# Kernel tuning notes

Measured on AMD Instinct MI355X. Metric: run time of the kernel, lower is better.

## Reference

```python
import jax, jax.numpy as jnp
import numpy as np

D_MODEL = 64     # input_dim // 4
D_INNER = 128    # expand * d_model
D_STATE = 16
D_CONV = 4
DT_RANK = 4      # ceil(d_model / 16)
EPS = 1e-5


def layernorm(x, g, b):
    m = x.mean(-1, keepdims=True)
    v = x.var(-1, keepdims=True)
    return (x - m) * jax.lax.rsqrt(v + EPS) * g + b


def mamba(u, W_in, W_conv, b_conv, W_xproj, W_dt, b_dt, A_log, Dp, W_out):
    # u: [B, L, d_model]
    B, L, _ = u.shape
    xz = u @ W_in.T                              # [B, L, 2*d_inner]
    xi, z = xz[..., :D_INNER], xz[..., D_INNER:]
    # depthwise causal conv1d over L
    xp = jnp.pad(xi, ((0, 0), (D_CONV - 1, 0), (0, 0)))
    xc = b_conv + sum(xp[:, k:k + L, :] * W_conv[:, k] for k in range(D_CONV))
    xc = jax.nn.silu(xc)                         # [B, L, d_inner]
    proj = xc @ W_xproj.T                        # [B, L, dt_rank + 2*d_state]
    dtp = proj[..., :DT_RANK]
    Bm = proj[..., DT_RANK:DT_RANK + D_STATE]    # [B, L, d_state]
    Cm = proj[..., DT_RANK + D_STATE:]           # [B, L, d_state]
    dt = jax.nn.softplus(dtp @ W_dt.T + b_dt)    # [B, L, d_inner]
    A = -jnp.exp(A_log)                          # [d_inner, d_state]
    dA = jnp.exp(dt[..., None] * A)              # [B, L, d_inner, d_state]
    dBx = (dt * xc)[..., None] * Bm[:, :, None, :]

    def step(h, t):
        dA_t, dBx_t, C_t = t
        h = dA_t * h + dBx_t                     # [B, d_inner, d_state]
        return h, jnp.einsum('bds,bs->bd', h, C_t)

    h0 = jnp.zeros((B, D_INNER, D_STATE), u.dtype)
    _, ys = jax.lax.scan(step, h0, (dA.transpose(1, 0, 2, 3),
                                    dBx.transpose(1, 0, 2, 3),
                                    Cm.transpose(1, 0, 2)))
    y = ys.transpose(1, 0, 2) + Dp * xc          # [B, L, d_inner]
    y = y * jax.nn.silu(z)
    return y @ W_out.T                           # [B, L, d_model]


def _forward(x, x1, x2, x3, g1, be1, g2, be2, g3, be3, g4, be4, skip_scale,
             W_in, W_conv, b_conv, W_xproj, W_dt, b_dt, A_log, D, W_out):
    Bb, C = x.shape[:2]
    img_dims = x2.shape[2:]
    mparams = (W_in, W_conv, b_conv, W_xproj, W_dt, b_dt, A_log, D, W_out)

    def branch(inp, g, b):
        xf = inp.reshape(Bb, C, -1).transpose(0, 2, 1)   # [B, L, C]
        xn = layernorm(xf, g, b)
        return mamba(xn, *mparams) + skip_scale * xn

    x_mamba = jnp.concatenate([branch(x, g1, be1), branch(x1, g2, be2),
                               branch(x2, g3, be3), branch(x3, g4, be4)], axis=2)
    out = x_mamba.transpose(0, 2, 1).reshape(Bb, 4 * C, *img_dims)
    return out


def setup_inputs():
    key = jax.random.key(0)
    ks = jax.random.split(key, 12)
    f = lambda k, shp, s=1.0: jax.random.normal(k, shp, dtype=jnp.float32) * s
    inp = {
        'x': f(ks[0], (8, 64, 32, 32)),
        'x1': f(ks[1], (8, 64, 32, 32)),
        'x2': f(ks[2], (8, 64, 32, 32)),
        'x3': f(ks[3], (8, 64, 32, 32)),
        'g1': jnp.ones(64), 'be1': jnp.zeros(64),
        'g2': jnp.ones(64), 'be2': jnp.zeros(64),
        'g3': jnp.ones(64), 'be3': jnp.zeros(64),
        'g4': jnp.ones(64), 'be4': jnp.zeros(64),
        'skip_scale': jnp.ones((1,), jnp.float32),
        'W_in': f(ks[4], (2 * D_INNER, D_MODEL), 0.1),
        'W_conv': f(ks[5], (D_INNER, D_CONV), 0.3),
        'b_conv': jnp.zeros(D_INNER),
        'W_xproj': f(ks[6], (DT_RANK + 2 * D_STATE, D_INNER), 0.1),
        'W_dt': f(ks[7], (D_INNER, DT_RANK), 0.1),
        'b_dt': f(ks[8], (D_INNER,), 0.1),
        'A_log': jnp.log(jnp.tile(jnp.arange(1, D_STATE + 1, dtype=jnp.float32), (D_INNER, 1))),
        'D': jnp.ones(D_INNER),
        'W_out': f(ks[9], (D_MODEL, D_INNER), 0.1),
    }
    return inp


def reference(x, x1, x2, x3, g1, be1, g2, be2, g3, be3, g4, be4, skip_scale,
              W_in, W_conv, b_conv, W_xproj, W_dt, b_dt, A_log, D, W_out):
    return _forward(x, x1, x2, x3, g1, be1, g2, be2, g3, be3, g4, be4, skip_scale,
                    W_in, W_conv, b_conv, W_xproj, W_dt, b_dt, A_log, D, W_out)
```

## Files before the change

kernel.cpp:

```cpp
#include <hip/hip_runtime.h>
#include <hip/hip_bf16.h>

#define L2E 1.4426950408889634f
#define LN2 0.6931471805599453f

__device__ __forceinline__ float fexp2(float x) { return __builtin_amdgcn_exp2f(x); }
__device__ __forceinline__ float flog2(float x) { return __builtin_amdgcn_logf(x); }
__device__ __forceinline__ int uniform(int x) { return __builtin_amdgcn_readfirstlane(x); }
__device__ __forceinline__ float sigmoidf_(float v) { return 1.f / (1.f + fexp2(-v * L2E)); }
__device__ __forceinline__ float softplusf_(float t) {
    return (t > 20.f) ? t : LN2 * flog2(1.f + fexp2(t * L2E));
}

constexpr size_t O_M   = 0;
constexpr size_t O_RS  = 32768;
constexpr size_t O_G   = 65536;
constexpr size_t O_Z   = 4259840;
constexpr size_t O_XC  = 8454144;
constexpr size_t O_BM  = 12648448;
constexpr size_t O_CM  = 13172736;
constexpr size_t O_DTP = 13697024;
constexpr size_t O_HP  = 13828096;

__global__ __launch_bounds__(256) void k1_ln_inproj(
    const float* __restrict__ x0, const float* __restrict__ x1,
    const float* __restrict__ x2, const float* __restrict__ x3,
    const float* __restrict__ win,
    const float* __restrict__ g1, const float* __restrict__ be1,
    const float* __restrict__ g2, const float* __restrict__ be2,
    const float* __restrict__ g3, const float* __restrict__ be3,
    const float* __restrict__ g4, const float* __restrict__ be4,
    float* __restrict__ ws)
{
    __shared__ float sX[64 * 68];
    __shared__ float sW[64 * 68];
    __shared__ float sM[64], sR[64];
    int bid = blockIdx.x;
    int seq = bid >> 6, jb = (bid >> 4) & 3, pb = bid & 15;
    int branch = seq >> 3, b = seq & 7;
    int tid = threadIdx.x;
    int lane = tid & 63;
    int wq = uniform(tid >> 6);
    const float* xin = (branch==0)?x0:(branch==1)?x1:(branch==2)?x2:x3;
    const float* gam = (branch==0)?g1:(branch==1)?g2:(branch==2)?g3:g4;
    const float* bet = (branch==0)?be1:(branch==1)?be2:(branch==2)?be3:be4;
    const float* xb = xin + (size_t)b * 65536;

#pragma unroll
    for (int r = 0; r < 16; ++r) {
        int row = r * 4 + wq;
        sX[row * 68 + lane] = xb[(size_t)row * 1024 + pb * 64 + lane];
        sW[lane * 68 + row] = win[(size_t)(jb * 64 + row) * 64 + lane];
    }
    __syncthreads();
    if (tid < 64) {
        float sum = 0.f, sq = 0.f;
#pragma unroll
        for (int c = 0; c < 64; ++c) {
            float v = sX[c * 68 + tid];
            sum += v; sq += v * v;
        }
        float mean = sum * (1.f/64.f);
        float var  = sq * (1.f/64.f) - mean * mean;
        float rs   = rsqrtf(var + 1e-5f);
        sM[tid] = mean; sR[tid] = rs;
        if (jb == 0) {
            ws[O_M  + (size_t)seq * 1024 + pb * 64 + tid] = mean;
            ws[O_RS + (size_t)seq * 1024 + pb * 64 + tid] = rs;
        }
    }
    __syncthreads();
#pragma unroll
    for (int r = 0; r < 16; ++r) {
        int c = r * 4 + wq;
        float v = sX[c * 68 + lane];
        sX[c * 68 + lane] = (v - sM[lane]) * sR[lane] * gam[c] + bet[c];
    }
    __syncthreads();
    int jt = tid >> 4, pt = tid & 15;
    float acc[4][4];
#pragma unroll
    for (int i = 0; i < 4; ++i)
#pragma unroll
        for (int j = 0; j < 4; ++j) acc[i][j] = 0.f;
    for (int c = 0; c < 64; ++c) {
        float4 wv = *(const float4*)&sW[c * 68 + jt * 4];
        float4 xv = *(const float4*)&sX[c * 68 + pt * 4];
        float w[4] = {wv.x, wv.y, wv.z, wv.w};
        float x[4] = {xv.x, xv.y, xv.z, xv.w};
#pragma unroll
        for (int i = 0; i < 4; ++i)
#pragma unroll
            for (int j = 0; j < 4; ++j) acc[i][j] += w[i] * x[j];
    }
    int p0 = pb * 64 + pt * 4;
    float* xi = ws + O_G + (size_t)seq * 131072;
    float* zz = ws + O_Z + (size_t)seq * 131072;
#pragma unroll
    for (int ji = 0; ji < 4; ++ji) {
        int j = jb * 64 + jt * 4 + ji;
        float4 v = make_float4(acc[ji][0], acc[ji][1], acc[ji][2], acc[ji][3]);
        if (j < 128) *(float4*)&xi[(size_t)j * 1024 + p0] = v;
        else         *(float4*)&zz[(size_t)(j - 128) * 1024 + p0] = v;
    }
}

__global__ __launch_bounds__(256) void k2_conv_proj(
    const float* __restrict__ wconv, const float* __restrict__ bconv,
    const float* __restrict__ wxp, float* __restrict__ ws)
{
    __shared__ float sX[128 * 68];
    int bid = blockIdx.x;
    int seq = bid >> 4, ptile = bid & 15;
    int tid = threadIdx.x;
    int lane = tid & 63;
    int wq = uniform(tid >> 6);
    int p0 = ptile * 64;
    int p  = p0 + lane;

    const float* xirow = ws + O_G  + (size_t)seq * 131072;
    float*       xcrow = ws + O_XC + (size_t)seq * 131072;

#pragma unroll 4
    for (int r = 0; r < 32; ++r) {
        int d = r * 4 + wq;
        const float* row = xirow + (size_t)d * 1024;
        int gp = p0 - 3 + lane;
        sX[d * 68 + lane] = (gp >= 0) ? row[gp] : 0.f;
        if (lane < 3) sX[d * 68 + 64 + lane] = row[p0 + 61 + lane];
    }
    __syncthreads();

#pragma unroll 2
    for (int dd = 0; dd < 32; ++dd) {
        int d = wq * 32 + dd;
        float4 wc = *(const float4*)&wconv[d * 4];
        float v = bconv[d];
        float* rowl = &sX[d * 68];
        v += rowl[lane + 0] * wc.x;
        v += rowl[lane + 1] * wc.y;
        v += rowl[lane + 2] * wc.z;
        v += rowl[lane + 3] * wc.w;
        v = v * sigmoidf_(v);
        xcrow[(size_t)d * 1024 + p] = v;
        rowl[lane + 3] = v;
    }
    __syncthreads();

    int j0 = uniform(wq * 9);
    const float* __restrict__ w0 = wxp + (size_t)j0 * 128;
    float acc[9];
#pragma unroll
    for (int jj = 0; jj < 9; ++jj) acc[jj] = 0.f;
#pragma unroll 4
    for (int d = 0; d < 128; ++d) {
        float xcv = sX[d * 68 + 3 + lane];
#pragma unroll
        for (int jj = 0; jj < 9; ++jj)
            acc[jj] += w0[jj * 128 + d] * xcv;
    }

    float* Bm = ws + O_BM + (size_t)seq * 16384;
    float* Cm = ws + O_CM + (size_t)seq * 16384;
#pragma unroll
    for (int jj = 0; jj < 9; ++jj) {
        int j = j0 + jj;
        float t = acc[jj];
        if (j < 4)       ws[O_DTP + ((size_t)seq * 1024 + p) * 4 + j] = t;
        else if (j < 20) Bm[(size_t)(j - 4)  * 1024 + p] = t;
        else             Cm[(size_t)(j - 20) * 1024 + p] = t;
    }
}

__device__ __forceinline__ void k3_preload(const float* wdt, const float* bdt,
                                           const float* alog, int d0, int s0,
                                           float4& wdt0, float4& wdt1, float& bdt0, float& bdt1,
                                           float* a2)
{
    wdt0 = *(const float4*)(wdt + d0 * 4);
    wdt1 = *(const float4*)(wdt + (d0 + 1) * 4);
    bdt0 = bdt[d0]; bdt1 = bdt[d0 + 1];
    float4 a0 = *(const float4*)(alog + d0 * 16 + s0);
    float4 a1 = *(const float4*)(alog + (d0 + 1) * 16 + s0);
    a2[0] = -fexp2(a0.x * L2E) * L2E; a2[1] = -fexp2(a0.y * L2E) * L2E;
    a2[2] = -fexp2(a0.z * L2E) * L2E; a2[3] = -fexp2(a0.w * L2E) * L2E;
    a2[4] = -fexp2(a1.x * L2E) * L2E; a2[5] = -fexp2(a1.y * L2E) * L2E;
    a2[6] = -fexp2(a1.z * L2E) * L2E; a2[7] = -fexp2(a1.w * L2E) * L2E;
}

__global__ __launch_bounds__(256) void k3a_scan(const float* __restrict__ wdt,
                                                const float* __restrict__ bdt,
                                                const float* __restrict__ alog,
                                                float* __restrict__ ws)
{
    __shared__ float sXC[128 * 33];
    __shared__ __align__(16) float sB[32 * 16];
    __shared__ __align__(16) float sDtp[32 * 4];
    int bid = blockIdx.x;
    int seq = bid >> 5, ch = bid & 31;
    int lb = ch * 32;
    int tid = threadIdx.x;
    int d0 = (tid >> 2) * 2, s0 = (tid & 3) * 4;

    float4 wdt0, wdt1; float bdt0, bdt1; float a2[8];
    k3_preload(wdt, bdt, alog, d0, s0, wdt0, wdt1, bdt0, bdt1, a2);

    const float* xcg = ws + O_XC + (size_t)seq * 131072;
    const float* Bmg = ws + O_BM + (size_t)seq * 16384;
    for (int i = tid; i < 4096; i += 256) {
        int d = i >> 5, li = i & 31;
        sXC[d * 33 + li] = xcg[(size_t)d * 1024 + lb + li];
    }
    for (int i = tid; i < 512; i += 256) {
        int s = i >> 5, li = i & 31;
        sB[li * 16 + s] = Bmg[(size_t)s * 1024 + lb + li];
    }
    if (tid < 128) sDtp[tid] = ws[O_DTP + ((size_t)seq * 1024 + lb + (tid >> 2)) * 4 + (tid & 3)];
    __syncthreads();

    float h[8];
#pragma unroll
    for (int i = 0; i < 8; ++i) h[i] = 0.f;
    float sdt0 = 0.f, sdt1 = 0.f;
    for (int li = 0; li < 32; ++li) {
        float4 q = *(const float4*)&sDtp[li * 4];
        float dt0 = softplusf_(bdt0 + q.x*wdt0.x + q.y*wdt0.y + q.z*wdt0.z + q.w*wdt0.w);
        float dt1 = softplusf_(bdt1 + q.x*wdt1.x + q.y*wdt1.y + q.z*wdt1.z + q.w*wdt1.w);
        float xc0 = sXC[d0 * 33 + li], xc1 = sXC[(d0 + 1) * 33 + li];
        float dx0 = dt0 * xc0, dx1 = dt1 * xc1;
        float4 Bv = *(const float4*)&sB[li * 16 + s0];
        float bv[4] = {Bv.x, Bv.y, Bv.z, Bv.w};
        sdt0 += dt0; sdt1 += dt1;
#pragma unroll
        for (int ss = 0; ss < 4; ++ss) {
            float e0 = fexp2(dt0 * a2[ss]);
            h[ss] = e0 * h[ss] + dx0 * bv[ss];
            float e1 = fexp2(dt1 * a2[4 + ss]);
            h[4 + ss] = e1 * h[4 + ss] + dx1 * bv[ss];
        }
    }
    float* hp = ws + O_HP + (size_t)(seq * 32 + ch) * 4096;
#pragma unroll
    for (int ss = 0; ss < 4; ++ss) {
        hp[d0 * 16 + s0 + ss]            = fexp2(a2[ss] * sdt0);
        hp[(d0 + 1) * 16 + s0 + ss]      = fexp2(a2[4 + ss] * sdt1);
        hp[2048 + d0 * 16 + s0 + ss]     = h[ss];
        hp[2048 + (d0 + 1) * 16 + s0 + ss] = h[4 + ss];
    }
}

__global__ __launch_bounds__(256) void k3b_compose(float* __restrict__ ws)
{
    int seq = blockIdx.x;
    int tid = threadIdx.x;
    int d0 = (tid >> 2) * 2, s0 = (tid & 3) * 4;
    int i0 = d0 * 16 + s0, i1 = (d0 + 1) * 16 + s0;
    float h[8];
#pragma unroll
    for (int i = 0; i < 8; ++i) h[i] = 0.f;
    float* hpb = ws + O_HP + (size_t)seq * 32 * 4096;
    for (int c = 0; c < 32; ++c) {
        float* hp = hpb + (size_t)c * 4096;
        float4 P0 = *(const float4*)&hp[i0];
        float4 P1 = *(const float4*)&hp[i1];
        float4 E0 = *(const float4*)&hp[2048 + i0];
        float4 E1 = *(const float4*)&hp[2048 + i1];
        *(float4*)&hp[i0] = make_float4(h[0], h[1], h[2], h[3]);
        *(float4*)&hp[i1] = make_float4(h[4], h[5], h[6], h[7]);
        h[0] = P0.x * h[0] + E0.x; h[1] = P0.y * h[1] + E0.y;
        h[2] = P0.z * h[2] + E0.z; h[3] = P0.w * h[3] + E0.w;
        h[4] = P1.x * h[4] + E1.x; h[5] = P1.y * h[5] + E1.y;
        h[6] = P1.z * h[6] + E1.z; h[7] = P1.w * h[7] + E1.w;
    }
}

__global__ __launch_bounds__(256) void k3c_scan_y(const float* __restrict__ wdt,
                                                  const float* __restrict__ bdt,
                                                  const float* __restrict__ alog,
                                                  float* __restrict__ ws)
{
    __shared__ float sXC[128 * 33];
    __shared__ float sY[128 * 33];
    __shared__ __align__(16) float sB[32 * 16];
    __shared__ __align__(16) float sC[32 * 16];
    __shared__ __align__(16) float sDtp[32 * 4];
    int bid = blockIdx.x;
    int seq = bid >> 5, ch = bid & 31;
    int lb = ch * 32;
    int tid = threadIdx.x;
    int sq = tid & 3;
    int d0 = (tid >> 2) * 2, s0 = sq * 4;

    float4 wdt0, wdt1; float bdt0, bdt1; float a2[8];
    k3_preload(wdt, bdt, alog, d0, s0, wdt0, wdt1, bdt0, bdt1, a2);

    const float* xcg = ws + O_XC + (size_t)seq * 131072;
    const float* Bmg = ws + O_BM + (size_t)seq * 16384;
    const float* Cmg = ws + O_CM + (size_t)seq * 16384;
    float*       gg  = ws + O_G  + (size_t)seq * 131072;
    for (int i = tid; i < 4096; i += 256) {
        int d = i >> 5, li = i & 31;
        sXC[d * 33 + li] = xcg[(size_t)d * 1024 + lb + li];
    }
    for (int i = tid; i < 512; i += 256) {
        int s = i >> 5, li = i & 31;
        sB[li * 16 + s] = Bmg[(size_t)s * 1024 + lb + li];
        sC[li * 16 + s] = Cmg[(size_t)s * 1024 + lb + li];
    }
    if (tid < 128) sDtp[tid] = ws[O_DTP + ((size_t)seq * 1024 + lb + (tid >> 2)) * 4 + (tid & 3)];

    const float* hp = ws + O_HP + (size_t)(seq * 32 + ch) * 4096;
    float4 H0 = *(const float4*)&hp[d0 * 16 + s0];
    float4 H1 = *(const float4*)&hp[(d0 + 1) * 16 + s0];
    float h[8] = {H0.x, H0.y, H0.z, H0.w, H1.x, H1.y, H1.z, H1.w};
    __syncthreads();

    for (int li = 0; li < 32; ++li) {
        float4 q = *(const float4*)&sDtp[li * 4];
        float dt0 = softplusf_(bdt0 + q.x*wdt0.x + q.y*wdt0.y + q.z*wdt0.z + q.w*wdt0.w);
        float dt1 = softplusf_(bdt1 + q.x*wdt1.x + q.y*wdt1.y + q.z*wdt1.z + q.w*wdt1.w);
        float xc0 = sXC[d0 * 33 + li], xc1 = sXC[(d0 + 1) * 33 + li];
        float dx0 = dt0 * xc0, dx1 = dt1 * xc1;
        float4 Bv = *(const float4*)&sB[li * 16 + s0];
        float4 Cv = *(const float4*)&sC[li * 16 + s0];
        float bv[4] = {Bv.x, Bv.y, Bv.z, Bv.w};
        float cv[4] = {Cv.x, Cv.y, Cv.z, Cv.w};
        float acc0 = 0.f, acc1 = 0.f;
#pragma unroll
        for (int ss = 0; ss < 4; ++ss) {
            float e0 = fexp2(dt0 * a2[ss]);
            h[ss] = e0 * h[ss] + dx0 * bv[ss];
            acc0 += h[ss] * cv[ss];
            float e1 = fexp2(dt1 * a2[4 + ss]);
            h[4 + ss] = e1 * h[4 + ss] + dx1 * bv[ss];
            acc1 += h[4 + ss] * cv[ss];
        }
        acc0 += __shfl_xor(acc0, 1); acc0 += __shfl_xor(acc0, 2);
        acc1 += __shfl_xor(acc1, 1); acc1 += __shfl_xor(acc1, 2);
        if (sq == 0) {
            sY[d0 * 33 + li]       = acc0;
            sY[(d0 + 1) * 33 + li] = acc1;
        }
    }
    __syncthreads();
    for (int i = tid; i < 4096; i += 256) {
        int d = i >> 5, li = i & 31;
        gg[(size_t)d * 1024 + lb + li] = sY[d * 33 + li];
    }
}

__global__ __launch_bounds__(256) void k4_out(
    const float* __restrict__ x0, const float* __restrict__ x1,
    const float* __restrict__ x2, const float* __restrict__ x3,
    const float* __restrict__ g1, const float* __restrict__ be1,
    const float* __restrict__ g2, const float* __restrict__ be2,
    const float* __restrict__ g3, const float* __restrict__ be3,
    const float* __restrict__ g4, const float* __restrict__ be4,
    const float* __restrict__ dpar, const float* __restrict__ woutp,
    const float* __restrict__ skipp, const float* __restrict__ ws,
    float* __restrict__ out)
{
    __shared__ float sG[64 * 68];
    __shared__ float sW[64 * 68];
    int bid = blockIdx.x;
    int seq = bid >> 4, pb = bid & 15;
    int branch = seq >> 3, b = seq & 7;
    int tid = threadIdx.x;
    int lane = tid & 63;
    int wq = uniform(tid >> 6);
    int ct = tid >> 4, pt = tid & 15;

    const float* ys = ws + O_G  + (size_t)seq * 131072;
    const float* zz = ws + O_Z  + (size_t)seq * 131072;
    const float* xc = ws + O_XC + (size_t)seq * 131072;

    float acc[4][4];
#pragma unroll
    for (int i = 0; i < 4; ++i)
#pragma unroll
        for (int j = 0; j < 4; ++j) acc[i][j] = 0.f;

    for (int hf = 0; hf < 2; ++hf) {
#pragma unroll
        for (int r = 0; r < 16; ++r) {
            int row = r * 4 + wq;
            sW[lane * 68 + row] = woutp[(size_t)row * 128 + hf * 64 + lane];
            int d = hf * 64 + row;
            size_t off = (size_t)d * 1024 + pb * 64 + lane;
            float yv = ys[off], zv = zz[off], xcv = xc[off];
            sG[row * 68 + lane] = (yv + dpar[d] * xcv) * (zv * sigmoidf_(zv));
        }
        __syncthreads();
        for (int dl = 0; dl < 64; ++dl) {
            float4 wv = *(const float4*)&sW[dl * 68 + ct * 4];
            float4 gv = *(const float4*)&sG[dl * 68 + pt * 4];
            float w[4] = {wv.x, wv.y, wv.z, wv.w};
            float g[4] = {gv.x, gv.y, gv.z, gv.w};
#pragma unroll
            for (int i = 0; i < 4; ++i)
#pragma unroll
                for (int j = 0; j < 4; ++j) acc[i][j] += w[i] * g[j];
        }
        __syncthreads();
    }

    const float* xin = (branch==0)?x0:(branch==1)?x1:(branch==2)?x2:x3;
    const float* gam = (branch==0)?g1:(branch==1)?g2:(branch==2)?g3:g4;
    const float* bet = (branch==0)?be1:(branch==1)?be2:(branch==2)?be3:be4;
    const float* xb = xin + (size_t)b * 65536;
    int p0 = pb * 64 + pt * 4;
    float skipv = skipp[0];
    float4 m4 = *(const float4*)&ws[O_M  + (size_t)seq * 1024 + p0];
    float4 r4 = *(const float4*)&ws[O_RS + (size_t)seq * 1024 + p0];
    float mm[4] = {m4.x, m4.y, m4.z, m4.w};
    float rr[4] = {r4.x, r4.y, r4.z, r4.w};
#pragma unroll
    for (int ci = 0; ci < 4; ++ci) {
        int c = ct * 4 + ci;
        float4 xv = *(const float4*)&xb[(size_t)c * 1024 + p0];
        float xvv[4] = {xv.x, xv.y, xv.z, xv.w};
        float gc = gam[c], bc = bet[c];
        float o[4];
#pragma unroll
        for (int pi = 0; pi < 4; ++pi) {
            float xn = (xvv[pi] - mm[pi]) * rr[pi] * gc + bc;
            o[pi] = acc[ci][pi] + skipv * xn;
        }
        *(float4*)&out[((size_t)b * 256 + branch * 64 + c) * 1024 + p0] =
            make_float4(o[0], o[1], o[2], o[3]);
    }
}

extern "C" void kernel_launch(void* const* d_in, const int* in_sizes, int n_in,
                              void* d_out, int out_size, void* d_ws, size_t ws_size,
                              hipStream_t stream) {
    float* ws = (float*)d_ws;
    auto f = [&](int i) { return (const float*)d_in[i]; };
    hipLaunchKernelGGL(k1_ln_inproj, dim3(2048), dim3(256), 0, stream,
        f(0), f(1), f(2), f(3), f(13),
        f(4), f(5), f(6), f(7), f(8), f(9), f(10), f(11), ws);
    hipLaunchKernelGGL(k2_conv_proj, dim3(512), dim3(256), 0, stream,
        f(14), f(15), f(16), ws);
    hipLaunchKernelGGL(k3a_scan, dim3(1024), dim3(256), 0, stream, f(17), f(18), f(19), ws);
    hipLaunchKernelGGL(k3b_compose, dim3(32), dim3(256), 0, stream, ws);
    hipLaunchKernelGGL(k3c_scan_y, dim3(1024), dim3(256), 0, stream, f(17), f(18), f(19), ws);
    hipLaunchKernelGGL(k4_out, dim3(512), dim3(256), 0, stream,
        f(0), f(1), f(2), f(3),
        f(4), f(5), f(6), f(7), f(8), f(9), f(10), f(11),
        f(20), f(21), f(12), ws, (float*)d_out);
}
```

Before: 232.6 us.

## Fuse scan-output and out-projection kernels, widen compose grid, stage xproj weights in LDS

The chunked scan output kernel now also applies the D skip, the SiLU(z) gating, the out-projection and the layernorm residual directly from shared memory. This removes the y round-trip through global memory and one kernel launch. The compose kernel is spread over 256 blocks with one state element per thread and prefetches the next chunk, so it no longer runs on only 32 blocks. The conv/proj kernel stages W_xproj transposed in LDS and reads it with vector loads. The cost is that each of the 1024 fused blocks reloads the full 32KB W_out into LDS, and the larger LDS footprint may reduce occupancy.

```diff
diff --git a/kernel.cpp b/kernel.cpp
--- a/kernel.cpp
+++ b/kernel.cpp
@@ -110,6 +110,7 @@
     const float* __restrict__ wxp, float* __restrict__ ws)
 {
     __shared__ float sX[128 * 68];
+    __shared__ float sWr[4 * 128 * 12];
     int bid = blockIdx.x;
     int seq = bid >> 4, ptile = bid & 15;
     int tid = threadIdx.x;
@@ -117,6 +118,7 @@
     int wq = uniform(tid >> 6);
     int p0 = ptile * 64;
     int p  = p0 + lane;
+    int j0 = wq * 9;
 
     const float* xirow = ws + O_G  + (size_t)seq * 131072;
     float*       xcrow = ws + O_XC + (size_t)seq * 131072;
@@ -128,6 +130,14 @@
         int gp = p0 - 3 + lane;
         sX[d * 68 + lane] = (gp >= 0) ? row[gp] : 0.f;
         if (lane < 3) sX[d * 68 + 64 + lane] = row[p0 + 61 + lane];
+    }
+#pragma unroll
+    for (int jj = 0; jj < 9; ++jj) {
+#pragma unroll
+        for (int half = 0; half < 2; ++half) {
+            int d = half * 64 + lane;
+            sWr[(wq * 128 + d) * 12 + jj] = wxp[(size_t)(j0 + jj) * 128 + d];
+        }
     }
     __syncthreads();
 
@@ -147,17 +157,21 @@
     }
     __syncthreads();
 
-    int j0 = uniform(wq * 9);
-    const float* __restrict__ w0 = wxp + (size_t)j0 * 128;
     float acc[9];
 #pragma unroll
     for (int jj = 0; jj < 9; ++jj) acc[jj] = 0.f;
 #pragma unroll 4
     for (int d = 0; d < 128; ++d) {
         float xcv = sX[d * 68 + 3 + lane];
-#pragma unroll
-        for (int jj = 0; jj < 9; ++jj)
-            acc[jj] += w0[jj * 128 + d] * xcv;
+        const float* wr = &sWr[(wq * 128 + d) * 12];
+        float4 wA = *(const float4*)wr;
+        float4 wB = *(const float4*)(wr + 4);
+        float  w8 = wr[8];
+        acc[0] += wA.x * xcv; acc[1] += wA.y * xcv;
+        acc[2] += wA.z * xcv; acc[3] += wA.w * xcv;
+        acc[4] += wB.x * xcv; acc[5] += wB.y * xcv;
+        acc[6] += wB.z * xcv; acc[7] += wB.w * xcv;
+        acc[8] += w8 * xcv;
     }
 
     float* Bm = ws + O_BM + (size_t)seq * 16384;
@@ -251,41 +265,44 @@
 
 __global__ __launch_bounds__(256) void k3b_compose(float* __restrict__ ws)
 {
-    int seq = blockIdx.x;
-    int tid = threadIdx.x;
-    int d0 = (tid >> 2) * 2, s0 = (tid & 3) * 4;
-    int i0 = d0 * 16 + s0, i1 = (d0 + 1) * 16 + s0;
-    float h[8];
-#pragma unroll
-    for (int i = 0; i < 8; ++i) h[i] = 0.f;
+    int seq = blockIdx.x >> 3, dg = blockIdx.x & 7;
+    int idx = dg * 256 + threadIdx.x;
+    float h = 0.f;
     float* hpb = ws + O_HP + (size_t)seq * 32 * 4096;
+    float P = hpb[idx];
+    float E = hpb[2048 + idx];
     for (int c = 0; c < 32; ++c) {
         float* hp = hpb + (size_t)c * 4096;
-        float4 P0 = *(const float4*)&hp[i0];
-        float4 P1 = *(const float4*)&hp[i1];
-        float4 E0 = *(const float4*)&hp[2048 + i0];
-        float4 E1 = *(const float4*)&hp[2048 + i1];
-        *(float4*)&hp[i0] = make_float4(h[0], h[1], h[2], h[3]);
-        *(float4*)&hp[i1] = make_float4(h[4], h[5], h[6], h[7]);
-        h[0] = P0.x * h[0] + E0.x; h[1] = P0.y * h[1] + E0.y;
-        h[2] = P0.z * h[2] + E0.z; h[3] = P0.w * h[3] + E0.w;
-        h[4] = P1.x * h[4] + E1.x; h[5] = P1.y * h[5] + E1.y;
-        h[6] = P1.z * h[6] + E1.z; h[7] = P1.w * h[7] + E1.w;
-    }
-}
-
-__global__ __launch_bounds__(256) void k3c_scan_y(const float* __restrict__ wdt,
-                                                  const float* __restrict__ bdt,
-                                                  const float* __restrict__ alog,
-                                                  float* __restrict__ ws)
+        float Pn = 0.f, En = 0.f;
+        if (c < 31) { Pn = hp[4096 + idx]; En = hp[4096 + 2048 + idx]; }
+        hp[idx] = h;
+        h = P * h + E;
+        P = Pn; E = En;
+    }
+}
+
+__global__ __launch_bounds__(256) void k3cd(
+    const float* __restrict__ wdt, const float* __restrict__ bdt,
+    const float* __restrict__ alog,
+    const float* __restrict__ x0, const float* __restrict__ x1,
+    const float* __restrict__ x2, const float* __restrict__ x3,
+    const float* __restrict__ g1, const float* __restrict__ be1,
+    const float* __restrict__ g2, const float* __restrict__ be2,
+    const float* __restrict__ g3, const float* __restrict__ be3,
+    const float* __restrict__ g4, const float* __restrict__ be4,
+    const float* __restrict__ dpar, const float* __restrict__ woutp,
+    const float* __restrict__ skipp, float* __restrict__ ws,
+    float* __restrict__ out)
 {
     __shared__ float sXC[128 * 33];
-    __shared__ float sY[128 * 33];
+    __shared__ __align__(16) float sY[128 * 36];
+    __shared__ float sWt[128 * 66];
     __shared__ __align__(16) float sB[32 * 16];
     __shared__ __align__(16) float sC[32 * 16];
     __shared__ __align__(16) float sDtp[32 * 4];
     int bid = blockIdx.x;
     int seq = bid >> 5, ch = bid & 31;
+    int branch = seq >> 3, b = seq & 7;
     int lb = ch * 32;
     int tid = threadIdx.x;
     int sq = tid & 3;
@@ -297,7 +314,6 @@
     const float* xcg = ws + O_XC + (size_t)seq * 131072;
     const float* Bmg = ws + O_BM + (size_t)seq * 16384;
     const float* Cmg = ws + O_CM + (size_t)seq * 16384;
-    float*       gg  = ws + O_G  + (size_t)seq * 131072;
     for (int i = tid; i < 4096; i += 256) {
         int d = i >> 5, li = i & 31;
         sXC[d * 33 + li] = xcg[(size_t)d * 1024 + lb + li];
@@ -308,6 +324,10 @@
         sC[li * 16 + s] = Cmg[(size_t)s * 1024 + lb + li];
     }
     if (tid < 128) sDtp[tid] = ws[O_DTP + ((size_t)seq * 1024 + lb + (tid >> 2)) * 4 + (tid & 3)];
+    for (int i = tid; i < 64 * 128; i += 256) {
+        int c = i >> 7, d = i & 127;
+        sWt[d * 66 + c] = woutp[i];
+    }
 
     const float* hp = ws + O_HP + (size_t)(seq * 32 + ch) * 4096;
     float4 H0 = *(const float4*)&hp[d0 * 16 + s0];
@@ -338,86 +358,54 @@
         acc0 += __shfl_xor(acc0, 1); acc0 += __shfl_xor(acc0, 2);
         acc1 += __shfl_xor(acc1, 1); acc1 += __shfl_xor(acc1, 2);
         if (sq == 0) {
-            sY[d0 * 33 + li]       = acc0;
-            sY[(d0 + 1) * 33 + li] = acc1;
-        }
-    }
-    __syncthreads();
+            sY[d0 * 36 + li]       = acc0;
+            sY[(d0 + 1) * 36 + li] = acc1;
+        }
+    }
+    __syncthreads();
+
+    const float* zzg = ws + O_Z + (size_t)seq * 131072;
     for (int i = tid; i < 4096; i += 256) {
         int d = i >> 5, li = i & 31;
-        gg[(size_t)d * 1024 + lb + li] = sY[d * 33 + li];
-    }
-}
-
-__global__ __launch_bounds__(256) void k4_out(
-    const float* __restrict__ x0, const float* __restrict__ x1,
-    const float* __restrict__ x2, const float* __restrict__ x3,
-    const float* __restrict__ g1, const float* __restrict__ be1,
-    const float* __restrict__ g2, const float* __restrict__ be2,
-    const float* __restrict__ g3, const float* __restrict__ be3,
-    const float* __restrict__ g4, const float* __restrict__ be4,
-    const float* __restrict__ dpar, const float* __restrict__ woutp,
-    const float* __restrict__ skipp, const float* __restrict__ ws,
-    float* __restrict__ out)
-{
-    __shared__ float sG[64 * 68];
-    __shared__ float sW[64 * 68];
-    int bid = blockIdx.x;
-    int seq = bid >> 4, pb = bid & 15;
-    int branch = seq >> 3, b = seq & 7;
-    int tid = threadIdx.x;
-    int lane = tid & 63;
-    int wq = uniform(tid >> 6);
-    int ct = tid >> 4, pt = tid & 15;
-
-    const float* ys = ws + O_G  + (size_t)seq * 131072;
-    const float* zz = ws + O_Z  + (size_t)seq * 131072;
-    const float* xc = ws + O_XC + (size_t)seq * 131072;
-
-    float acc[4][4];
-#pragma unroll
-    for (int i = 0; i < 4; ++i)
+        float zv = zzg[(size_t)d * 1024 + lb + li];
+        float yv = sY[d * 36 + li];
+        float xcv = sXC[d * 33 + li];
+        sY[d * 36 + li] = (yv + dpar[d] * xcv) * (zv * sigmoidf_(zv));
+    }
+    __syncthreads();
+
+    int ctt = tid >> 3;
+    int ptq = tid & 7;
+    int c0 = ctt * 2;
+    float acc[2][4];
+#pragma unroll
+    for (int i = 0; i < 2; ++i)
 #pragma unroll
         for (int j = 0; j < 4; ++j) acc[i][j] = 0.f;
-
-    for (int hf = 0; hf < 2; ++hf) {
-#pragma unroll
-        for (int r = 0; r < 16; ++r) {
-            int row = r * 4 + wq;
-            sW[lane * 68 + row] = woutp[(size_t)row * 128 + hf * 64 + lane];
-            int d = hf * 64 + row;
-            size_t off = (size_t)d * 1024 + pb * 64 + lane;
-            float yv = ys[off], zv = zz[off], xcv = xc[off];
-            sG[row * 68 + lane] = (yv + dpar[d] * xcv) * (zv * sigmoidf_(zv));
-        }
-        __syncthreads();
-        for (int dl = 0; dl < 64; ++dl) {
-            float4 wv = *(const float4*)&sW[dl * 68 + ct * 4];
-            float4 gv = *(const float4*)&sG[dl * 68 + pt * 4];
-            float w[4] = {wv.x, wv.y, wv.z, wv.w};
-            float g[4] = {gv.x, gv.y, gv.z, gv.w};
-#pragma unroll
-            for (int i = 0; i < 4; ++i)
-#pragma unroll
-                for (int j = 0; j < 4; ++j) acc[i][j] += w[i] * g[j];
-        }
-        __syncthreads();
+#pragma unroll 4
+    for (int d = 0; d < 128; ++d) {
+        float2 wv = *(const float2*)&sWt[d * 66 + c0];
+        float4 gv = *(const float4*)&sY[d * 36 + ptq * 4];
+        acc[0][0] += wv.x * gv.x; acc[0][1] += wv.x * gv.y;
+        acc[0][2] += wv.x * gv.z; acc[0][3] += wv.x * gv.w;
+        acc[1][0] += wv.y * gv.x; acc[1][1] += wv.y * gv.y;
+        acc[1][2] += wv.y * gv.z; acc[1][3] += wv.y * gv.w;
     }
 
     const float* xin = (branch==0)?x0:(branch==1)?x1:(branch==2)?x2:x3;
     const float* gam = (branch==0)?g1:(branch==1)?g2:(branch==2)?g3:g4;
     const float* bet = (branch==0)?be1:(branch==1)?be2:(branch==2)?be3:be4;
     const float* xb = xin + (size_t)b * 65536;
-    int p0 = pb * 64 + pt * 4;
+    int pp = lb + ptq * 4;
     float skipv = skipp[0];
-    float4 m4 = *(const float4*)&ws[O_M  + (size_t)seq * 1024 + p0];
-    float4 r4 = *(const float4*)&ws[O_RS + (size_t)seq * 1024 + p0];
+    float4 m4 = *(const float4*)&ws[O_M  + (size_t)seq * 1024 + pp];
+    float4 r4 = *(const float4*)&ws[O_RS + (size_t)seq * 1024 + pp];
     float mm[4] = {m4.x, m4.y, m4.z, m4.w};
     float rr[4] = {r4.x, r4.y, r4.z, r4.w};
 #pragma unroll
-    for (int ci = 0; ci < 4; ++ci) {
-        int c = ct * 4 + ci;
-        float4 xv = *(const float4*)&xb[(size_t)c * 1024 + p0];
+    for (int ci = 0; ci < 2; ++ci) {
+        int c = c0 + ci;
+        float4 xv = *(const float4*)&xb[(size_t)c * 1024 + pp];
         float xvv[4] = {xv.x, xv.y, xv.z, xv.w};
         float gc = gam[c], bc = bet[c];
         float o[4];
@@ -426,7 +414,7 @@
             float xn = (xvv[pi] - mm[pi]) * rr[pi] * gc + bc;
             o[pi] = acc[ci][pi] + skipv * xn;
         }
-        *(float4*)&out[((size_t)b * 256 + branch * 64 + c) * 1024 + p0] =
+        *(float4*)&out[((size_t)b * 256 + branch * 64 + c) * 1024 + pp] =
             make_float4(o[0], o[1], o[2], o[3]);
     }
 }
@@ -442,9 +430,9 @@
     hipLaunchKernelGGL(k2_conv_proj, dim3(512), dim3(256), 0, stream,
         f(14), f(15), f(16), ws);
     hipLaunchKernelGGL(k3a_scan, dim3(1024), dim3(256), 0, stream, f(17), f(18), f(19), ws);
-    hipLaunchKernelGGL(k3b_compose, dim3(32), dim3(256), 0, stream, ws);
-    hipLaunchKernelGGL(k3c_scan_y, dim3(1024), dim3(256), 0, stream, f(17), f(18), f(19), ws);
-    hipLaunchKernelGGL(k4_out, dim3(512), dim3(256), 0, stream,
+    hipLaunchKernelGGL(k3b_compose, dim3(256), dim3(256), 0, stream, ws);
+    hipLaunchKernelGGL(k3cd, dim3(1024), dim3(256), 0, stream,
+        f(17), f(18), f(19),
         f(0), f(1), f(2), f(3),
         f(4), f(5), f(6), f(7), f(8), f(9), f(10), f(11),
         f(20), f(21), f(12), ws, (float*)d_out);
```

New measurement: 229.3 us. About the same (-1.4%).
